# Performance work log

Hardware: AMD Instinct MI355X
Metric: run time of the kernel (lower is better)

Reference implementation:

```python
import jax, jax.numpy as jnp
import numpy as np

N, M = 50000, 2048          # nodes, observations
E, O = 512, 256             # in_features_embed, in_features_obs
EPS = 1e-6


def setup_inputs() -> dict:
    key = jax.random.key(0)
    k1, k2, k3, k4, k5 = jax.random.split(key, 5)
    scale_e = 1.0 / np.sqrt(E)
    scale_o = 1.0 / np.sqrt(O)
    return {
        "node_feature": jax.random.normal(k1, (N, E), dtype=jnp.float32),
        "obs_feature": jax.random.normal(k2, (M, O), dtype=jnp.float32),
        # nn.Linear weights, stored as [out, in] like torch
        "W_q": jax.random.normal(k3, (E, E), dtype=jnp.float32) * scale_e,
        "W_k": jax.random.normal(k4, (E, O), dtype=jnp.float32) * scale_o,
        "W_v": jax.random.normal(k5, (E, O), dtype=jnp.float32) * scale_o,
        "ln_gamma": jnp.ones((E,), dtype=jnp.float32),
        "ln_beta": jnp.zeros((E,), dtype=jnp.float32),
    }


def layer_norm(x, gamma, beta, eps=EPS):
    mu = jnp.mean(x, axis=-1, keepdims=True)
    var = jnp.mean(jnp.square(x - mu), axis=-1, keepdims=True)
    return (x - mu) * jax.lax.rsqrt(var + eps) * gamma + beta


def reference(node_feature, obs_feature, W_q, W_k, W_v, ln_gamma, ln_beta):
    # projections (torch Linear: x @ W.T)
    q = node_feature @ W_q.T            # [N, E]
    k = obs_feature @ W_k.T             # [M, E]
    v = obs_feature @ W_v.T             # [M, E]
    # un-normalized cross-attention (no softmax), original association
    attn = q @ k.T                      # [N, M]
    out = attn @ v                      # [N, E]
    return layer_norm(out + node_feature, ln_gamma, ln_beta)
```

## Files before the change

### kernel.cpp

```cpp
#include <hip/hip_runtime.h>
#include <hip/hip_bf16.h>

#define NROWS 50000
#define MOBS  2048
#define EDIM  512
#define ODIM  256

typedef short s16x8 __attribute__((ext_vector_type(8)));
typedef float f32x4 __attribute__((ext_vector_type(4)));

__device__ __forceinline__ unsigned short f32_to_bf16(float f) {
    unsigned int u = __float_as_uint(f);
    u += 0x7fffu + ((u >> 16) & 1u);
    return (unsigned short)(u >> 16);
}

__global__ __launch_bounds__(256) void gp_fused(const float* __restrict__ obs,
                                                const float* __restrict__ Wq,
                                                const float* __restrict__ Wk,
                                                float* __restrict__ G,
                                                float* __restrict__ P) {
    __shared__ float SA[16][68];
    __shared__ float SB[16][68];
    const float *A, *B;
    float* C;
    int lda, ldb, k_lo, k_hi;
    const int bz = blockIdx.z;
    if (bz < 16) {
        if (blockIdx.y >= 4) return;
        A = obs; B = obs; C = G; lda = ODIM; ldb = ODIM;
        k_lo = bz * (MOBS / 16); k_hi = k_lo + MOBS / 16;
    } else {
        A = Wq; B = Wk; C = P; lda = EDIM; ldb = ODIM;
        k_lo = (bz - 16) * (EDIM / 4); k_hi = k_lo + EDIM / 4;
    }
    const int t  = threadIdx.x;
    const int tx = t & 15, ty = t >> 4;
    const int i0 = blockIdx.y * 64, j0 = blockIdx.x * 64;

    float acc[4][4];
#pragma unroll
    for (int a = 0; a < 4; ++a)
#pragma unroll
        for (int b = 0; b < 4; ++b) acc[a][b] = 0.f;

    for (int k0 = k_lo; k0 < k_hi; k0 += 16) {
#pragma unroll
        for (int r = 0; r < 4; ++r) {
            int idx = t + 256 * r;
            int mm = idx & 63, kk2 = idx >> 6;
            SA[kk2][mm] = A[(size_t)(k0 + kk2) * lda + i0 + mm];
        }
#pragma unroll
        for (int r = 0; r < 4; ++r) {
            int idx = t + 256 * r;
            int jj = idx & 63, kk2 = idx >> 6;
            SB[kk2][jj] = B[(size_t)(k0 + kk2) * ldb + j0 + jj];
        }
        __syncthreads();
#pragma unroll
        for (int kk2 = 0; kk2 < 16; ++kk2) {
            float4 a4 = *(const float4*)&SA[kk2][ty * 4];
            float4 b4 = *(const float4*)&SB[kk2][tx * 4];
            float av[4] = {a4.x, a4.y, a4.z, a4.w};
            float bv[4] = {b4.x, b4.y, b4.z, b4.w};
#pragma unroll
            for (int a = 0; a < 4; ++a)
#pragma unroll
                for (int b = 0; b < 4; ++b) acc[a][b] += av[a] * bv[b];
        }
        __syncthreads();
    }
#pragma unroll
    for (int a = 0; a < 4; ++a)
#pragma unroll
        for (int b = 0; b < 4; ++b)
            atomicAdd(&C[(size_t)(i0 + ty * 4 + a) * ODIM + j0 + tx * 4 + b],
                      acc[a][b]);
}

template <int TA, int TB, int SPLIT, int FRAG>
__global__ __launch_bounds__(256) void sgemm4(const float* __restrict__ A,
                                              const float* __restrict__ B,
                                              void* __restrict__ Cv,
                                              int NN, int KK, int lda, int ldb) {
    __shared__ float SA[16][68];
    __shared__ float SB[16][68];
    const int t  = threadIdx.x;
    const int tx = t & 15, ty = t >> 4;
    const int i0 = blockIdx.y * 64, j0 = blockIdx.x * 64;
    int k_lo = 0, k_hi = KK;
    if (SPLIT > 1) { int ch = KK / SPLIT; k_lo = blockIdx.z * ch; k_hi = k_lo + ch; }

    float acc[4][4];
#pragma unroll
    for (int a = 0; a < 4; ++a)
#pragma unroll
        for (int b = 0; b < 4; ++b) acc[a][b] = 0.f;

    for (int k0 = k_lo; k0 < k_hi; k0 += 16) {
#pragma unroll
        for (int r = 0; r < 4; ++r) {
            int idx = t + 256 * r;
            int mm, kk2;
            if (TA) { mm = idx & 63; kk2 = idx >> 6; }
            else    { kk2 = idx & 15; mm = idx >> 4; }
            SA[kk2][mm] = TA ? A[(size_t)(k0 + kk2) * lda + i0 + mm]
                             : A[(size_t)(i0 + mm) * lda + k0 + kk2];
        }
#pragma unroll
        for (int r = 0; r < 4; ++r) {
            int idx = t + 256 * r;
            int jj, kk2;
            if (TB) { kk2 = idx & 15; jj = idx >> 4; }
            else    { jj = idx & 63; kk2 = idx >> 6; }
            SB[kk2][jj] = TB ? B[(size_t)(j0 + jj) * ldb + k0 + kk2]
                             : B[(size_t)(k0 + kk2) * ldb + j0 + jj];
        }
        __syncthreads();
#pragma unroll
        for (int kk2 = 0; kk2 < 16; ++kk2) {
            float4 a4 = *(const float4*)&SA[kk2][ty * 4];
            float4 b4 = *(const float4*)&SB[kk2][tx * 4];
            float av[4] = {a4.x, a4.y, a4.z, a4.w};
            float bv[4] = {b4.x, b4.y, b4.z, b4.w};
#pragma unroll
            for (int a = 0; a < 4; ++a)
#pragma unroll
                for (int b = 0; b < 4; ++b) acc[a][b] += av[a] * bv[b];
        }
        __syncthreads();
    }

    if (FRAG) {
        unsigned short* C = (unsigned short*)Cv;
#pragma unroll
        for (int a = 0; a < 4; ++a)
#pragma unroll
            for (int b = 0; b < 4; ++b) {
                int i = i0 + ty * 4 + a;
                int j = j0 + tx * 4 + b;
                float v = acc[a][b] + (i == j ? 1.f : 0.f);
                int f = j >> 4, lr = j & 15, kk = i >> 5, lk = (i >> 3) & 3;
                C[((size_t)((f * 16 + kk) * 64 + lk * 16 + lr)) * 8 + (i & 7)] =
                    f32_to_bf16(v);
            }
    } else if (SPLIT > 1) {
        float* C = (float*)Cv;
#pragma unroll
        for (int a = 0; a < 4; ++a)
#pragma unroll
            for (int b = 0; b < 4; ++b)
                atomicAdd(&C[(size_t)(i0 + ty * 4 + a) * NN + j0 + tx * 4 + b],
                          acc[a][b]);
    } else {
        float* C = (float*)Cv;
#pragma unroll
        for (int a = 0; a < 4; ++a) {
            float4 o = make_float4(acc[a][0], acc[a][1], acc[a][2], acc[a][3]);
            *(float4*)&C[(size_t)(i0 + ty * 4 + a) * NN + j0 + tx * 4] = o;
        }
    }
}

__global__ __launch_bounds__(512, 4) void gemm_mfma_ln(
    const float* __restrict__ node, const unsigned short* __restrict__ Uf,
    const float* __restrict__ gamma, const float* __restrict__ beta,
    float* __restrict__ out) {
    __shared__ unsigned short As[64 * 512];
    float* lds_s  = (float*)As;
    float* lds_q  = (float*)As + 512;
    float* lds_mu = (float*)As + 1024;
    float* lds_rs = (float*)As + 1088;

    const int t  = threadIdx.x;
    const int w  = t >> 6;
    const int l  = t & 63;
    const int lr = l & 15;
    const int lk = l >> 4;
    const int m0 = blockIdx.x * 64;

#pragma unroll
    for (int it = 0; it < 8; ++it) {
        int row = it * 8 + w;
        int gr = m0 + row;
        if (gr > NROWS - 1) gr = NROWS - 1;
        const float4* p = (const float4*)(node + (size_t)gr * EDIM + l * 8);
        float4 f0 = p[0], f1 = p[1];
        s16x8 av;
        av[0] = (short)f32_to_bf16(f0.x); av[1] = (short)f32_to_bf16(f0.y);
        av[2] = (short)f32_to_bf16(f0.z); av[3] = (short)f32_to_bf16(f0.w);
        av[4] = (short)f32_to_bf16(f1.x); av[5] = (short)f32_to_bf16(f1.y);
        av[6] = (short)f32_to_bf16(f1.z); av[7] = (short)f32_to_bf16(f1.w);
        int byte = row * 1024 + ((l * 16) ^ ((row & 7) << 4));
        *(s16x8*)((char*)As + byte) = av;
    }
    __syncthreads();

    f32x4 acc[4][4];
#pragma unroll
    for (int mi = 0; mi < 4; ++mi)
#pragma unroll
        for (int ni = 0; ni < 4; ++ni)
            acc[mi][ni] = (f32x4){0.f, 0.f, 0.f, 0.f};

    const unsigned short* bw = Uf + (size_t)w * 32768 + (size_t)l * 8;

    s16x8 bfr[2][4];
#pragma unroll
    for (int ni = 0; ni < 4; ++ni)
        bfr[0][ni] = *(const s16x8*)(bw + (size_t)ni * 8192);

#pragma unroll
    for (int kk = 0; kk < 16; ++kk) {
        const int cur = kk & 1, nxt = cur ^ 1;
        if (kk < 15) {
#pragma unroll
            for (int ni = 0; ni < 4; ++ni)
                bfr[nxt][ni] =
                    *(const s16x8*)(bw + (size_t)ni * 8192 + (kk + 1) * 512);
        }
        s16x8 afr[4];
#pragma unroll
        for (int mi = 0; mi < 4; ++mi) {
            int row = mi * 16 + lr;
            int byte = row * 1024 + ((kk * 64 + lk * 16) ^ ((row & 7) << 4));
            afr[mi] = *(const s16x8*)((const char*)As + byte);
        }
#pragma unroll
        for (int mi = 0; mi < 4; ++mi)
#pragma unroll
            for (int ni = 0; ni < 4; ++ni)
                acc[mi][ni] = __builtin_amdgcn_mfma_f32_16x16x32_bf16(
                    afr[mi], bfr[cur][ni], acc[mi][ni], 0, 0, 0);
    }

    __syncthreads();

#pragma unroll
    for (int mi = 0; mi < 4; ++mi) {
#pragma unroll
        for (int j = 0; j < 4; ++j) {
            float s = 0.f, q = 0.f;
#pragma unroll
            for (int ni = 0; ni < 4; ++ni) {
                float v = acc[mi][ni][j];
                s += v; q += v * v;
            }
#pragma unroll
            for (int off = 1; off < 16; off <<= 1) {
                s += __shfl_xor(s, off);
                q += __shfl_xor(q, off);
            }
            if (lr == 0) {
                int rl = mi * 16 + lk * 4 + j;
                lds_s[w * 64 + rl] = s;
                lds_q[w * 64 + rl] = q;
            }
        }
    }
    __syncthreads();
    if (t < 64) {
        float s = 0.f, q = 0.f;
#pragma unroll
        for (int ww = 0; ww < 8; ++ww) {
            s += lds_s[ww * 64 + t];
            q += lds_q[ww * 64 + t];
        }
        float mu  = s * (1.f / (float)EDIM);
        float var = q * (1.f / (float)EDIM) - mu * mu;
        lds_mu[t] = mu;
        lds_rs[t] = rsqrtf(var + 1e-6f);
    }
    __syncthreads();

    const int n0 = w * 64;
    float gv[4], bv[4];
#pragma unroll
    for (int ni = 0; ni < 4; ++ni) {
        int c = n0 + ni * 16 + lr;
        gv[ni] = gamma[c];
        bv[ni] = beta[c];
    }

#pragma unroll
    for (int mi = 0; mi < 4; ++mi) {
#pragma unroll
        for (int j = 0; j < 4; ++j) {
            int rl = mi * 16 + lk * 4 + j;
            int gr = m0 + rl;
            if (gr < NROWS) {
                float mu = lds_mu[rl], rs = lds_rs[rl];
                float* op = out + (size_t)gr * EDIM + n0 + lr;
#pragma unroll
                for (int ni = 0; ni < 4; ++ni)
                    op[ni * 16] = (acc[mi][ni][j] - mu) * rs * gv[ni] + bv[ni];
            }
        }
    }
}

extern "C" void kernel_launch(void* const* d_in, const int* in_sizes, int n_in,
                              void* d_out, int out_size, void* d_ws, size_t ws_size,
                              hipStream_t stream) {
    const float* node  = (const float*)d_in[0];
    const float* obs   = (const float*)d_in[1];
    const float* Wq    = (const float*)d_in[2];
    const float* Wk    = (const float*)d_in[3];
    const float* Wv    = (const float*)d_in[4];
    const float* gamma = (const float*)d_in[5];
    const float* beta  = (const float*)d_in[6];
    float* out = (float*)d_out;

    float* ws = (float*)d_ws;
    float*          G  = ws;
    float*          P  = G  + ODIM * ODIM;
    float*          PG = P  + EDIM * ODIM;
    unsigned short* Uf = (unsigned short*)(PG + EDIM * ODIM);

    hipMemsetAsync((void*)G, 0,
                   (ODIM * ODIM + 2 * EDIM * ODIM) * sizeof(float), stream);

    gp_fused<<<dim3(4, 8, 20), 256, 0, stream>>>(obs, Wq, Wk, G, P);
    sgemm4<0, 0, 2, 0><<<dim3(4, 8, 2), 256, 0, stream>>>(P, G, PG, ODIM, ODIM, ODIM, ODIM);
    sgemm4<0, 1, 1, 1><<<dim3(8, 8, 1), 256, 0, stream>>>(PG, Wv, Uf, EDIM, ODIM, ODIM, ODIM);
    gemm_mfma_ln<<<dim3((NROWS + 63) / 64), 512, 0, stream>>>(node, Uf, gamma, beta, out);
}
```

Baseline: 129.6 us.

## Pre-convert node features to fragment-ordered bf16 in the prologue kernel; stream from global

The fp32 to bf16 conversion of node_feature moves out of the final GEMM+LayerNorm kernel and into extra blocks of the small prologue kernel. Those blocks write a bf16 buffer already laid out in MFMA fragment order. The final kernel then reads A fragments straight from global memory with no LDS staging or barrier, and uses a 2x8 wave tile instead of 4x4. This removes LDS traffic and the conversion from the critical kernel and overlaps it with the small GEMMs. The cost is an extra 51 MB write and read of the bf16 copy, plus heavier reuse of B from global or cache.

```diff
diff --git a/kernel.cpp b/kernel.cpp
--- a/kernel.cpp
+++ b/kernel.cpp
@@ -1,10 +1,11 @@
 #include <hip/hip_runtime.h>
 #include <hip/hip_bf16.h>
 
-#define NROWS 50000
-#define MOBS  2048
-#define EDIM  512
-#define ODIM  256
+#define NROWS  50000
+#define MOBS   2048
+#define EDIM   512
+#define ODIM   256
+#define NTILES 782
 
 typedef short s16x8 __attribute__((ext_vector_type(8)));
 typedef float f32x4 __attribute__((ext_vector_type(4)));
@@ -15,34 +16,60 @@
     return (unsigned short)(u >> 16);
 }
 
-__global__ __launch_bounds__(256) void gp_fused(const float* __restrict__ obs,
-                                                const float* __restrict__ Wq,
-                                                const float* __restrict__ Wk,
-                                                float* __restrict__ G,
-                                                float* __restrict__ P) {
+__global__ __launch_bounds__(256) void fused_pre(const float* __restrict__ node,
+                                                 const float* __restrict__ obs,
+                                                 const float* __restrict__ Wq,
+                                                 const float* __restrict__ Wk,
+                                                 unsigned short* __restrict__ Abf,
+                                                 float* __restrict__ G,
+                                                 float* __restrict__ P) {
+    const int b = blockIdx.x;
+    if (b >= 384) {
+        const int tile = b - 384;
+        const int t = threadIdx.x, w = t >> 6, l = t & 63;
+        const int kk = l >> 2, lk = l & 3;
+        unsigned short* tb = Abf + (size_t)tile * (64 * EDIM);
+#pragma unroll
+        for (int rr = 0; rr < 16; ++rr) {
+            int rit = rr * 4 + w;
+            int gr = tile * 64 + rit;
+            if (gr > NROWS - 1) gr = NROWS - 1;
+            const float4* p = (const float4*)(node + (size_t)gr * EDIM + l * 8);
+            float4 f0 = p[0], f1 = p[1];
+            s16x8 av;
+            av[0] = (short)f32_to_bf16(f0.x); av[1] = (short)f32_to_bf16(f0.y);
+            av[2] = (short)f32_to_bf16(f0.z); av[3] = (short)f32_to_bf16(f0.w);
+            av[4] = (short)f32_to_bf16(f1.x); av[5] = (short)f32_to_bf16(f1.y);
+            av[6] = (short)f32_to_bf16(f1.z); av[7] = (short)f32_to_bf16(f1.w);
+            int g = rit >> 4, lr = rit & 15;
+            *(s16x8*)(tb + ((size_t)((kk * 4 + g) * 64 + lk * 16 + lr)) * 8) = av;
+        }
+        return;
+    }
     __shared__ float SA[16][68];
     __shared__ float SB[16][68];
     const float *A, *B;
     float* C;
-    int lda, ldb, k_lo, k_hi;
-    const int bz = blockIdx.z;
-    if (bz < 16) {
-        if (blockIdx.y >= 4) return;
+    int lda, ldb, k_lo, k_hi, bx, by;
+    if (b < 256) {
+        bx = b & 3; by = (b >> 2) & 3; int bz = b >> 4;
         A = obs; B = obs; C = G; lda = ODIM; ldb = ODIM;
         k_lo = bz * (MOBS / 16); k_hi = k_lo + MOBS / 16;
     } else {
+        int i = b - 256;
+        bx = i & 3; by = (i >> 2) & 7; int bz = i >> 5;
         A = Wq; B = Wk; C = P; lda = EDIM; ldb = ODIM;
-        k_lo = (bz - 16) * (EDIM / 4); k_hi = k_lo + EDIM / 4;
+        k_lo = bz * (EDIM / 4); k_hi = k_lo + EDIM / 4;
     }
     const int t  = threadIdx.x;
     const int tx = t & 15, ty = t >> 4;
-    const int i0 = blockIdx.y * 64, j0 = blockIdx.x * 64;
+    const int i0 = by * 64, j0 = bx * 64;
 
     float acc[4][4];
 #pragma unroll
     for (int a = 0; a < 4; ++a)
 #pragma unroll
-        for (int b = 0; b < 4; ++b) acc[a][b] = 0.f;
+        for (int c2 = 0; c2 < 4; ++c2) acc[a][c2] = 0.f;
 
     for (int k0 = k_lo; k0 < k_hi; k0 += 16) {
 #pragma unroll
@@ -67,16 +94,16 @@
 #pragma unroll
             for (int a = 0; a < 4; ++a)
 #pragma unroll
-                for (int b = 0; b < 4; ++b) acc[a][b] += av[a] * bv[b];
+                for (int c2 = 0; c2 < 4; ++c2) acc[a][c2] += av[a] * bv[c2];
         }
         __syncthreads();
     }
 #pragma unroll
     for (int a = 0; a < 4; ++a)
 #pragma unroll
-        for (int b = 0; b < 4; ++b)
-            atomicAdd(&C[(size_t)(i0 + ty * 4 + a) * ODIM + j0 + tx * 4 + b],
-                      acc[a][b]);
+        for (int c2 = 0; c2 < 4; ++c2)
+            atomicAdd(&C[(size_t)(i0 + ty * 4 + a) * ODIM + j0 + tx * 4 + c2],
+                      acc[a][c2]);
 }
 
 template <int TA, int TB, int SPLIT, int FRAG>
@@ -163,137 +190,103 @@
     }
 }
 
-__global__ __launch_bounds__(512, 4) void gemm_mfma_ln(
-    const float* __restrict__ node, const unsigned short* __restrict__ Uf,
+__global__ __launch_bounds__(512, 4) void gemm_stream_ln(
+    const unsigned short* __restrict__ Abf, const unsigned short* __restrict__ Uf,
     const float* __restrict__ gamma, const float* __restrict__ beta,
     float* __restrict__ out) {
-    __shared__ unsigned short As[64 * 512];
-    float* lds_s  = (float*)As;
-    float* lds_q  = (float*)As + 512;
-    float* lds_mu = (float*)As + 1024;
-    float* lds_rs = (float*)As + 1088;
+    __shared__ float lds_s[4][64];
+    __shared__ float lds_q[4][64];
+    __shared__ float lds_mu[64];
+    __shared__ float lds_rs[64];
 
     const int t  = threadIdx.x;
     const int w  = t >> 6;
     const int l  = t & 63;
+    const int s  = w >> 2;
+    const int c  = w & 3;
     const int lr = l & 15;
     const int lk = l >> 4;
-    const int m0 = blockIdx.x * 64;
-
-#pragma unroll
-    for (int it = 0; it < 8; ++it) {
-        int row = it * 8 + w;
-        int gr = m0 + row;
-        if (gr > NROWS - 1) gr = NROWS - 1;
-        const float4* p = (const float4*)(node + (size_t)gr * EDIM + l * 8);
-        float4 f0 = p[0], f1 = p[1];
-        s16x8 av;
-        av[0] = (short)f32_to_bf16(f0.x); av[1] = (short)f32_to_bf16(f0.y);
-        av[2] = (short)f32_to_bf16(f0.z); av[3] = (short)f32_to_bf16(f0.w);
-        av[4] = (short)f32_to_bf16(f1.x); av[5] = (short)f32_to_bf16(f1.y);
-        av[6] = (short)f32_to_bf16(f1.z); av[7] = (short)f32_to_bf16(f1.w);
-        int byte = row * 1024 + ((l * 16) ^ ((row & 7) << 4));
-        *(s16x8*)((char*)As + byte) = av;
-    }
-    __syncthreads();
-
-    f32x4 acc[4][4];
-#pragma unroll
-    for (int mi = 0; mi < 4; ++mi)
-#pragma unroll
-        for (int ni = 0; ni < 4; ++ni)
+    const int tile = blockIdx.x;
+
+    const unsigned short* abase = Abf + (size_t)tile * (64 * EDIM) + (size_t)l * 8;
+    const unsigned short* bbase = Uf + (size_t)c * 65536 + (size_t)l * 8;
+
+    f32x4 acc[2][8];
+#pragma unroll
+    for (int mi = 0; mi < 2; ++mi)
+#pragma unroll
+        for (int ni = 0; ni < 8; ++ni)
             acc[mi][ni] = (f32x4){0.f, 0.f, 0.f, 0.f};
 
-    const unsigned short* bw = Uf + (size_t)w * 32768 + (size_t)l * 8;
-
-    s16x8 bfr[2][4];
-#pragma unroll
-    for (int ni = 0; ni < 4; ++ni)
-        bfr[0][ni] = *(const s16x8*)(bw + (size_t)ni * 8192);
-
 #pragma unroll
     for (int kk = 0; kk < 16; ++kk) {
-        const int cur = kk & 1, nxt = cur ^ 1;
-        if (kk < 15) {
-#pragma unroll
-            for (int ni = 0; ni < 4; ++ni)
-                bfr[nxt][ni] =
-                    *(const s16x8*)(bw + (size_t)ni * 8192 + (kk + 1) * 512);
-        }
-        s16x8 afr[4];
-#pragma unroll
-        for (int mi = 0; mi < 4; ++mi) {
-            int row = mi * 16 + lr;
-            int byte = row * 1024 + ((kk * 64 + lk * 16) ^ ((row & 7) << 4));
-            afr[mi] = *(const s16x8*)((const char*)As + byte);
-        }
-#pragma unroll
-        for (int mi = 0; mi < 4; ++mi)
-#pragma unroll
-            for (int ni = 0; ni < 4; ++ni)
+        s16x8 afr[2], bfr[8];
+#pragma unroll
+        for (int mi = 0; mi < 2; ++mi)
+            afr[mi] = *(const s16x8*)(abase + (size_t)(kk * 4 + 2 * s + mi) * 512);
+#pragma unroll
+        for (int ni = 0; ni < 8; ++ni)
+            bfr[ni] = *(const s16x8*)(bbase + (size_t)(ni * 16 + kk) * 512);
+#pragma unroll
+        for (int mi = 0; mi < 2; ++mi)
+#pragma unroll
+            for (int ni = 0; ni < 8; ++ni)
                 acc[mi][ni] = __builtin_amdgcn_mfma_f32_16x16x32_bf16(
-                    afr[mi], bfr[cur][ni], acc[mi][ni], 0, 0, 0);
-    }
-
-    __syncthreads();
-
-#pragma unroll
-    for (int mi = 0; mi < 4; ++mi) {
+                    afr[mi], bfr[ni], acc[mi][ni], 0, 0, 0);
+    }
+
+#pragma unroll
+    for (int mi = 0; mi < 2; ++mi) {
 #pragma unroll
         for (int j = 0; j < 4; ++j) {
-            float s = 0.f, q = 0.f;
-#pragma unroll
-            for (int ni = 0; ni < 4; ++ni) {
+            float sm = 0.f, q = 0.f;
+#pragma unroll
+            for (int ni = 0; ni < 8; ++ni) {
                 float v = acc[mi][ni][j];
-                s += v; q += v * v;
+                sm += v; q += v * v;
             }
 #pragma unroll
             for (int off = 1; off < 16; off <<= 1) {
-                s += __shfl_xor(s, off);
-                q += __shfl_xor(q, off);
+                sm += __shfl_xor(sm, off);
+                q  += __shfl_xor(q, off);
             }
             if (lr == 0) {
-                int rl = mi * 16 + lk * 4 + j;
-                lds_s[w * 64 + rl] = s;
-                lds_q[w * 64 + rl] = q;
+                int row = s * 32 + mi * 16 + lk * 4 + j;
+                lds_s[c][row] = sm;
+                lds_q[c][row] = q;
             }
         }
     }
     __syncthreads();
     if (t < 64) {
-        float s = 0.f, q = 0.f;
-#pragma unroll
-        for (int ww = 0; ww < 8; ++ww) {
-            s += lds_s[ww * 64 + t];
-            q += lds_q[ww * 64 + t];
-        }
-        float mu  = s * (1.f / (float)EDIM);
+        float sm = lds_s[0][t] + lds_s[1][t] + lds_s[2][t] + lds_s[3][t];
+        float q  = lds_q[0][t] + lds_q[1][t] + lds_q[2][t] + lds_q[3][t];
+        float mu  = sm * (1.f / (float)EDIM);
         float var = q * (1.f / (float)EDIM) - mu * mu;
         lds_mu[t] = mu;
         lds_rs[t] = rsqrtf(var + 1e-6f);
     }
     __syncthreads();
 
-    const int n0 = w * 64;
-    float gv[4], bv[4];
-#pragma unroll
-    for (int ni = 0; ni < 4; ++ni) {
-        int c = n0 + ni * 16 + lr;
-        gv[ni] = gamma[c];
-        bv[ni] = beta[c];
-    }
-
-#pragma unroll
-    for (int mi = 0; mi < 4; ++mi) {
+    float gv[8], bv[8];
+#pragma unroll
+    for (int ni = 0; ni < 8; ++ni) {
+        int col = c * 128 + ni * 16 + lr;
+        gv[ni] = gamma[col];
+        bv[ni] = beta[col];
+    }
+
+#pragma unroll
+    for (int mi = 0; mi < 2; ++mi) {
 #pragma unroll
         for (int j = 0; j < 4; ++j) {
-            int rl = mi * 16 + lk * 4 + j;
-            int gr = m0 + rl;
+            int row = s * 32 + mi * 16 + lk * 4 + j;
+            int gr = tile * 64 + row;
             if (gr < NROWS) {
-                float mu = lds_mu[rl], rs = lds_rs[rl];
-                float* op = out + (size_t)gr * EDIM + n0 + lr;
-#pragma unroll
-                for (int ni = 0; ni < 4; ++ni)
+                float mu = lds_mu[row], rs = lds_rs[row];
+                float* op = out + (size_t)gr * EDIM + c * 128 + lr;
+#pragma unroll
+                for (int ni = 0; ni < 8; ++ni)
                     op[ni * 16] = (acc[mi][ni][j] - mu) * rs * gv[ni] + bv[ni];
             }
         }
@@ -312,17 +305,17 @@
     const float* beta  = (const float*)d_in[6];
     float* out = (float*)d_out;
 
-    float* ws = (float*)d_ws;
-    float*          G  = ws;
-    float*          P  = G  + ODIM * ODIM;
-    float*          PG = P  + EDIM * ODIM;
+    unsigned short* Abf = (unsigned short*)d_ws;
+    float* G  = (float*)(Abf + (size_t)NTILES * 64 * EDIM);
+    float* P  = G  + ODIM * ODIM;
+    float* PG = P  + EDIM * ODIM;
     unsigned short* Uf = (unsigned short*)(PG + EDIM * ODIM);
 
     hipMemsetAsync((void*)G, 0,
                    (ODIM * ODIM + 2 * EDIM * ODIM) * sizeof(float), stream);
 
-    gp_fused<<<dim3(4, 8, 20), 256, 0, stream>>>(obs, Wq, Wk, G, P);
+    fused_pre<<<dim3(384 + NTILES), 256, 0, stream>>>(node, obs, Wq, Wk, Abf, G, P);
     sgemm4<0, 0, 2, 0><<<dim3(4, 8, 2), 256, 0, stream>>>(P, G, PG, ODIM, ODIM, ODIM, ODIM);
     sgemm4<0, 1, 1, 1><<<dim3(8, 8, 1), 256, 0, stream>>>(PG, Wv, Uf, EDIM, ODIM, ODIM, ODIM);
-    gemm_mfma_ln<<<dim3((NROWS + 63) / 64), 512, 0, stream>>>(node, Uf, gamma, beta, out);
-}
+    gemm_stream_ln<<<dim3(NTILES), 512, 0, stream>>>(Abf, Uf, gamma, beta, out);
+}
```

Measured after the change: 204.9 us. 58.1% more time.
